# Optimization experiments

Hardware: AMD Instinct MI355X
Metric: run time of the kernel (lower is better)

The kernel has to match this reference:

```python
import jax, jax.numpy as jnp
import numpy as np

B, L, D = 2, 1024, 768
K = 64            # window_size
MLP_HIDDEN = 128
DIFF_STEPS = 1
EPS = 1e-8        # torch F.cosine_similarity eps


def setup_inputs() -> dict:
    key = jax.random.key(0)
    ks = jax.random.split(key, 7)
    x = jax.random.normal(ks[0], (B, L, D), dtype=jnp.float32)
    alpha = jnp.asarray(0.1, dtype=jnp.float32)
    pos_emb = jax.random.normal(ks[1], (K, D), dtype=jnp.float32) * 0.02
    w1 = jax.random.normal(ks[2], (2 * D, MLP_HIDDEN), dtype=jnp.float32) * 0.02
    b1 = jnp.zeros((MLP_HIDDEN,), dtype=jnp.float32)
    w2 = jax.random.normal(ks[3], (MLP_HIDDEN, D), dtype=jnp.float32) * 0.02
    b2 = jnp.zeros((D,), dtype=jnp.float32)
    return {"x": x, "alpha": alpha, "pos_emb": pos_emb,
            "w1": w1, "b1": b1, "w2": w2, "b2": b2}


def reference(x, alpha, pos_emb, w1, b1, w2, b2):
    Bx, Lx, Dx = x.shape
    W = Lx - K + 1  # number of sliding windows
    # gather indices for unfold(2, K, 1): window w covers positions [w, w+K)
    idx = jnp.arange(W)[:, None] + jnp.arange(K)[None, :]  # [W, K]

    x_curr = x
    first_pre_energy = jnp.asarray(0.0, jnp.float32)
    final_post_energy = jnp.asarray(0.0, jnp.float32)
    total_update_norm = jnp.asarray(0.0, jnp.float32)
    total_cos_sim = jnp.asarray(0.0, jnp.float32)

    for step in range(DIFF_STEPS):
        windows = x_curr[:, idx, :]                 # [B, W, K, D]
        context = windows[:, :, :-1, :]             # [B, W, K-1, D]
        current = windows[:, :, -1, :]              # [B, W, D]
        pe = jnp.broadcast_to(pos_emb[: K - 1], (Bx, W, K - 1, Dx))
        mlp_in = jnp.concatenate([context, pe], axis=-1)        # [B, W, K-1, 2D]
        h = jax.nn.relu(jnp.einsum('bwkc,ch->bwkh', mlp_in, w1) + b1)
        pred = jnp.einsum('bwkh,hd->bwkd', h, w2) + b2          # [B, W, K-1, D]
        deltas = current[:, :, None, :] - pred                  # [B, W, K-1, D]
        mean_delta = deltas.mean(axis=2)                        # [B, W, D]
        update = -(alpha * mean_delta)                          # [B, W, D]
        x_next = x_curr.at[:, K - 1:, :].add(update)

        pre_energy = (mean_delta ** 2).sum(axis=-1).mean()
        up_norm = jnp.linalg.norm(update, axis=-1).mean()
        a = current
        b = current + update
        na = jnp.maximum(jnp.linalg.norm(a, axis=-1), EPS)
        nb = jnp.maximum(jnp.linalg.norm(b, axis=-1), EPS)
        cos_sim = ((a * b).sum(axis=-1) / (na * nb)).mean()

        if step == 0:
            first_pre_energy = pre_energy
        total_update_norm = total_update_norm + up_norm
        total_cos_sim = total_cos_sim + cos_sim
        x_curr = x_next
        alpha_val = jax.lax.stop_gradient(alpha)  # mirrors .item() detach
        post_energy = (1.0 - alpha_val) ** 2 * pre_energy
        if step == DIFF_STEPS - 1:
            final_post_energy = post_energy

    return (x_curr,
            first_pre_energy,
            final_post_energy,
            total_update_norm / DIFF_STEPS,
            total_cos_sim / DIFF_STEPS)
```

## Files before the change

### kernel.cpp

```cpp
#include <hip/hip_runtime.h>

constexpr int Bn = 2;
constexpr int Ln = 1024;
constexpr int Dn = 768;
constexpr int Hn = 128;
constexpr int KM1 = 63;
constexpr int Wn = 961;
constexpr int RB = 4;
constexpr int WB = 8;
constexpr int WCHUNKS = (Wn + WB - 1) / WB;
constexpr int NROW = Bn * Wn;
constexpr float EPSf = 1e-8f;

__device__ __forceinline__ float4 f4l(const float* p) { return *reinterpret_cast<const float4*>(p); }
__device__ __forceinline__ void f4s(float* p, float4 v) { *reinterpret_cast<float4*>(p) = v; }
__device__ __forceinline__ float4 f4fma(float s, float4 w, float4 a) {
    a.x = fmaf(s, w.x, a.x); a.y = fmaf(s, w.y, a.y);
    a.z = fmaf(s, w.z, a.z); a.w = fmaf(s, w.w, a.w);
    return a;
}

__global__ __launch_bounds__(512)
void k_gemm1(const float* __restrict__ x, const float* __restrict__ pos_emb,
             const float* __restrict__ w1, const float* __restrict__ b1,
             float* __restrict__ xw1, float* __restrict__ pew1,
             float* __restrict__ out)
{
    __shared__ float xs[RB * Dn];
    __shared__ float part[16 * RB * Hn];
    const int tid = threadIdx.x;
    const int h4 = tid & 31;
    const int ks = tid >> 5;
    const int blk = blockIdx.x;
    constexpr int NXB = (Bn * Ln) / RB;
    const bool isX = blk < NXB;
    const int peb = blk - NXB;

    const float* src = isX ? (x + blk * RB * Dn) : (pos_emb + peb * RB * Dn);
    const int nv = isX ? RB : min(RB, KM1 - peb * RB);

    for (int idx = tid; idx < nv * (Dn / 4); idx += 512)
        ((float4*)xs)[idx] = ((const float4*)src)[idx];
    __syncthreads();

    if (isX) {
        const int r0 = blk * RB;
        if ((r0 & (Ln - 1)) < KM1) {
            for (int idx = tid; idx < RB * (Dn / 4); idx += 512) {
                const int i = idx / (Dn / 4);
                const int r = r0 + i;
                if ((r & (Ln - 1)) < KM1)
                    ((float4*)out)[r * (Dn / 4) + (idx - i * (Dn / 4))] = ((const float4*)xs)[idx];
            }
        }
    }

    const int woff = isX ? 0 : Dn;
    float4 acc0 = make_float4(0.f, 0.f, 0.f, 0.f);
    float4 acc1 = acc0, acc2 = acc0, acc3 = acc0;
    const int cbase = ks * 48;
    for (int cc = 0; cc < 48; cc += 4) {
        const int c = cbase + cc;
        const float* wp = w1 + (woff + c) * Hn + 4 * h4;
        const float4 wv0 = f4l(wp);
        const float4 wv1 = f4l(wp + Hn);
        const float4 wv2 = f4l(wp + 2 * Hn);
        const float4 wv3 = f4l(wp + 3 * Hn);
        const float4 x0 = ((const float4*)xs)[(0 * Dn + c) >> 2];
        const float4 x1 = ((const float4*)xs)[(1 * Dn + c) >> 2];
        const float4 x2 = ((const float4*)xs)[(2 * Dn + c) >> 2];
        const float4 x3 = ((const float4*)xs)[(3 * Dn + c) >> 2];
        acc0 = f4fma(x0.x, wv0, acc0); acc0 = f4fma(x0.y, wv1, acc0);
        acc0 = f4fma(x0.z, wv2, acc0); acc0 = f4fma(x0.w, wv3, acc0);
        acc1 = f4fma(x1.x, wv0, acc1); acc1 = f4fma(x1.y, wv1, acc1);
        acc1 = f4fma(x1.z, wv2, acc1); acc1 = f4fma(x1.w, wv3, acc1);
        acc2 = f4fma(x2.x, wv0, acc2); acc2 = f4fma(x2.y, wv1, acc2);
        acc2 = f4fma(x2.z, wv2, acc2); acc2 = f4fma(x2.w, wv3, acc2);
        acc3 = f4fma(x3.x, wv0, acc3); acc3 = f4fma(x3.y, wv1, acc3);
        acc3 = f4fma(x3.z, wv2, acc3); acc3 = f4fma(x3.w, wv3, acc3);
    }
    ((float4*)part)[((ks * RB + 0) * Hn + 4 * h4) >> 2] = acc0;
    ((float4*)part)[((ks * RB + 1) * Hn + 4 * h4) >> 2] = acc1;
    ((float4*)part)[((ks * RB + 2) * Hn + 4 * h4) >> 2] = acc2;
    ((float4*)part)[((ks * RB + 3) * Hn + 4 * h4) >> 2] = acc3;
    __syncthreads();

    const int oi = tid >> 7;
    const int oh = tid & 127;
    float s = 0.f;
    #pragma unroll
    for (int k2 = 0; k2 < 16; ++k2)
        s += part[(k2 * RB + oi) * Hn + oh];
    if (isX) {
        xw1[(blk * RB + oi) * Hn + oh] = s;
    } else if (oi < nv) {
        pew1[(peb * RB + oi) * Hn + oh] = s + b1[oh];
    }
}

__global__ __launch_bounds__(256)
void k_fused(const float* __restrict__ x, const float* __restrict__ alpha_p,
             const float* __restrict__ w2, const float* __restrict__ b2,
             const float* __restrict__ xw1, const float* __restrict__ pew1,
             float* __restrict__ out, float* __restrict__ partial)
{
    __shared__ float xsl[(WB + KM1 - 1) * Hn];
    __shared__ float hsm[WB * Hn];
    __shared__ float4 red[4 * WB * 64];
    const int tid = threadIdx.x;
    int bid = blockIdx.x;
    const int dc = bid % 3; bid /= 3;
    const int chunk = bid % WCHUNKS;
    const int b = bid / WCHUNKS;
    const int w0 = chunk * WB;
    const int wcount = min(WB, Wn - w0);
    const int nrows = wcount + KM1 - 1;
    const float alpha = alpha_p[0];

    {
        const float4* src = (const float4*)(xw1 + (b * Ln + w0) * Hn);
        for (int idx = tid; idx < nrows * (Hn / 4); idx += 256)
            ((float4*)xsl)[idx] = src[idx];
    }
    __syncthreads();

    {
        const int w = tid >> 5;
        const int h4 = tid & 31;
        float4 s = make_float4(0.f, 0.f, 0.f, 0.f);
        const float* pp = pew1 + 4 * h4;
        #pragma unroll 7
        for (int k = 0; k < KM1; ++k) {
            const float4 xv = ((const float4*)xsl)[((w + k) * Hn + 4 * h4) >> 2];
            const float4 pv = f4l(pp + k * Hn);
            s.x += fmaxf(xv.x + pv.x, 0.f);
            s.y += fmaxf(xv.y + pv.y, 0.f);
            s.z += fmaxf(xv.z + pv.z, 0.f);
            s.w += fmaxf(xv.w + pv.w, 0.f);
        }
        const float sc = 1.0f / 63.0f;
        s.x *= sc; s.y *= sc; s.z *= sc; s.w *= sc;
        ((float4*)hsm)[(w * Hn + 4 * h4) >> 2] = s;
    }
    __syncthreads();

    const int d4 = tid & 63;
    const int hs = tid >> 6;
    float4 acc[WB];
    #pragma unroll
    for (int w = 0; w < WB; ++w) acc[w] = make_float4(0.f, 0.f, 0.f, 0.f);
    const int d = dc * 256 + d4 * 4;
    const int h0 = hs * 32;
    for (int hh = 0; hh < 32; ++hh) {
        const int h = h0 + hh;
        const float4 wv = f4l(w2 + h * Dn + d);
        #pragma unroll
        for (int w = 0; w < WB; ++w)
            acc[w] = f4fma(hsm[w * Hn + h], wv, acc[w]);
    }
    #pragma unroll
    for (int w = 0; w < WB; ++w)
        red[(hs * WB + w) * 64 + d4] = acc[w];
    __syncthreads();

    const int wloc = tid >> 5;
    float4 pp = make_float4(0.f, 0.f, 0.f, 0.f);
    if (wloc < wcount) {
        const int rowoff = (b * Ln + w0 + wloc + KM1) * Dn + dc * 256;
        #pragma unroll
        for (int j = 0; j < 2; ++j) {
            const int dp = (2 * tid + j) & 63;
            float4 sum = red[wloc * 64 + dp];
            #pragma unroll
            for (int k = 1; k < 4; ++k) {
                const float4 u = red[(k * WB + wloc) * 64 + dp];
                sum.x += u.x; sum.y += u.y; sum.z += u.z; sum.w += u.w;
            }
            const float4 bb = f4l(b2 + dc * 256 + dp * 4);
            const float4 xv = f4l(x + rowoff + dp * 4);
            float4 md;
            md.x = xv.x - (sum.x + bb.x);
            md.y = xv.y - (sum.y + bb.y);
            md.z = xv.z - (sum.z + bb.z);
            md.w = xv.w - (sum.w + bb.w);
            float4 nb;
            nb.x = fmaf(-alpha, md.x, xv.x);
            nb.y = fmaf(-alpha, md.y, xv.y);
            nb.z = fmaf(-alpha, md.z, xv.z);
            nb.w = fmaf(-alpha, md.w, xv.w);
            f4s(out + rowoff + dp * 4, nb);
            pp.x += md.x * md.x + md.y * md.y + md.z * md.z + md.w * md.w;
            pp.y += xv.x * xv.x + xv.y * xv.y + xv.z * xv.z + xv.w * xv.w;
            pp.z += xv.x * nb.x + xv.y * nb.y + xv.z * nb.z + xv.w * nb.w;
            pp.w += nb.x * nb.x + nb.y * nb.y + nb.z * nb.z + nb.w * nb.w;
        }
    }
    #pragma unroll
    for (int off = 16; off > 0; off >>= 1) {
        pp.x += __shfl_xor(pp.x, off);
        pp.y += __shfl_xor(pp.y, off);
        pp.z += __shfl_xor(pp.z, off);
        pp.w += __shfl_xor(pp.w, off);
    }
    if (((tid & 31) == 0) && wloc < wcount)
        f4s(partial + (dc * NROW + b * Wn + w0 + wloc) * 4, pp);
}

__global__ __launch_bounds__(1024)
void k_final(const float* __restrict__ partial, const float* __restrict__ alpha_p,
             float* __restrict__ out)
{
    __shared__ float sred[16][3];
    const int tid = threadIdx.x;
    float se = 0.f, sn = 0.f, sc = 0.f;
    for (int r = tid; r < NROW; r += 1024) {
        const float4 v0 = ((const float4*)partial)[r];
        const float4 v1 = ((const float4*)partial)[NROW + r];
        const float4 v2 = ((const float4*)partial)[2 * NROW + r];
        const float sq = v0.x + v1.x + v2.x;
        const float aa = v0.y + v1.y + v2.y;
        const float ab = v0.z + v1.z + v2.z;
        const float bb = v0.w + v1.w + v2.w;
        se += sq;
        sn += sqrtf(sq);
        sc += ab / (fmaxf(sqrtf(aa), EPSf) * fmaxf(sqrtf(bb), EPSf));
    }
    #pragma unroll
    for (int off = 32; off > 0; off >>= 1) {
        se += __shfl_down(se, off);
        sn += __shfl_down(sn, off);
        sc += __shfl_down(sc, off);
    }
    const int wv = tid >> 6, lane = tid & 63;
    if (lane == 0) { sred[wv][0] = se; sred[wv][1] = sn; sred[wv][2] = sc; }
    __syncthreads();
    if (tid == 0) {
        float te = 0.f, tn = 0.f, tc = 0.f;
        #pragma unroll
        for (int i = 0; i < 16; ++i) {
            te += sred[i][0]; tn += sred[i][1]; tc += sred[i][2];
        }
        const float alpha = alpha_p[0];
        const float inv = 1.0f / (float)NROW;
        const float pre = te * inv;
        const float om = 1.0f - alpha;
        const int base = Bn * Ln * Dn;
        out[base + 0] = pre;
        out[base + 1] = om * om * pre;
        out[base + 2] = alpha * tn * inv;
        out[base + 3] = tc * inv;
    }
}

extern "C" void kernel_launch(void* const* d_in, const int* in_sizes, int n_in,
                              void* d_out, int out_size, void* d_ws, size_t ws_size,
                              hipStream_t stream)
{
    const float* x       = (const float*)d_in[0];
    const float* alpha_p = (const float*)d_in[1];
    const float* pos_emb = (const float*)d_in[2];
    const float* w1      = (const float*)d_in[3];
    const float* b1      = (const float*)d_in[4];
    const float* w2      = (const float*)d_in[5];
    const float* b2      = (const float*)d_in[6];
    float* out = (float*)d_out;

    float* xw1     = (float*)d_ws;
    float* pew1    = xw1 + Bn * Ln * Hn;
    float* partial = pew1 + KM1 * Hn;

    const int nblkA = (Bn * Ln) / RB + (KM1 + RB - 1) / RB;
    k_gemm1<<<nblkA, 512, 0, stream>>>(x, pos_emb, w1, b1, xw1, pew1, out);
    k_fused<<<Bn * WCHUNKS * 3, 256, 0, stream>>>(x, alpha_p, w2, b2, xw1, pew1, out, partial);
    k_final<<<1, 1024, 0, stream>>>(partial, alpha_p, out);
}
```

Measured before the change: 107.9 us.

## Fuse final reduction into main kernel via atomics and last-block completion

Drops the separate single-block final reduction kernel. The fused kernel now accumulates the energy, norm and cosine sums with global atomics, and the last block to finish (found through an atomic counter) writes the scalar outputs. Each block now covers all three D chunks for 4 windows instead of one chunk for 8, and the hidden-mean stage is split across k-groups with a shared-memory reduction. This removes one launch and the partial buffer, at the cost of atomic contention, float non-determinism in the sums, and a tiny grid for the W2 stage.

```diff
diff --git a/kernel.cpp b/kernel.cpp
--- a/kernel.cpp
+++ b/kernel.cpp
@@ -7,9 +7,10 @@
 constexpr int KM1 = 63;
 constexpr int Wn = 961;
 constexpr int RB = 4;
-constexpr int WB = 8;
+constexpr int WB = 4;
 constexpr int WCHUNKS = (Wn + WB - 1) / WB;
 constexpr int NROW = Bn * Wn;
+constexpr int FGRID = Bn * WCHUNKS;
 constexpr float EPSf = 1e-8f;
 
 __device__ __forceinline__ float4 f4l(const float* p) { return *reinterpret_cast<const float4*>(p); }
@@ -24,7 +25,7 @@
 void k_gemm1(const float* __restrict__ x, const float* __restrict__ pos_emb,
              const float* __restrict__ w1, const float* __restrict__ b1,
              float* __restrict__ xw1, float* __restrict__ pew1,
-             float* __restrict__ out)
+             float* __restrict__ out, float* __restrict__ accum)
 {
     __shared__ float xs[RB * Dn];
     __shared__ float part[16 * RB * Hn];
@@ -35,6 +36,8 @@
     constexpr int NXB = (Bn * Ln) / RB;
     const bool isX = blk < NXB;
     const int peb = blk - NXB;
+
+    if (blk == 0 && tid < 5) accum[tid] = 0.0f;
 
     const float* src = isX ? (x + blk * RB * Dn) : (pos_emb + peb * RB * Dn);
     const int nv = isX ? RB : min(RB, KM1 - peb * RB);
@@ -102,16 +105,16 @@
 void k_fused(const float* __restrict__ x, const float* __restrict__ alpha_p,
              const float* __restrict__ w2, const float* __restrict__ b2,
              const float* __restrict__ xw1, const float* __restrict__ pew1,
-             float* __restrict__ out, float* __restrict__ partial)
+             float* __restrict__ out, float* __restrict__ accum)
 {
     __shared__ float xsl[(WB + KM1 - 1) * Hn];
     __shared__ float hsm[WB * Hn];
-    __shared__ float4 red[4 * WB * 64];
+    __shared__ float4 red[1024];
+    __shared__ int lastFlag;
+
     const int tid = threadIdx.x;
-    int bid = blockIdx.x;
-    const int dc = bid % 3; bid /= 3;
-    const int chunk = bid % WCHUNKS;
-    const int b = bid / WCHUNKS;
+    const int b = blockIdx.x / WCHUNKS;
+    const int chunk = blockIdx.x % WCHUNKS;
     const int w0 = chunk * WB;
     const int wcount = min(WB, Wn - w0);
     const int nrows = wcount + KM1 - 1;
@@ -125,59 +128,77 @@
     __syncthreads();
 
     {
+        const int kg = tid >> 5;
+        const int h4 = tid & 31;
+        float4 s[WB];
+        #pragma unroll
+        for (int w = 0; w < WB; ++w) s[w] = make_float4(0.f, 0.f, 0.f, 0.f);
+        for (int k = kg; k < KM1; k += 8) {
+            const float4 pv = f4l(pew1 + k * Hn + 4 * h4);
+            #pragma unroll
+            for (int w = 0; w < WB; ++w) {
+                const float4 xv = ((const float4*)xsl)[((w + k) * Hn >> 2) + h4];
+                s[w].x += fmaxf(xv.x + pv.x, 0.f);
+                s[w].y += fmaxf(xv.y + pv.y, 0.f);
+                s[w].z += fmaxf(xv.z + pv.z, 0.f);
+                s[w].w += fmaxf(xv.w + pv.w, 0.f);
+            }
+        }
+        #pragma unroll
+        for (int w = 0; w < WB; ++w)
+            red[(kg * WB + w) * 32 + h4] = s[w];
+    }
+    __syncthreads();
+    if (tid < WB * 32) {
         const int w = tid >> 5;
         const int h4 = tid & 31;
-        float4 s = make_float4(0.f, 0.f, 0.f, 0.f);
-        const float* pp = pew1 + 4 * h4;
-        #pragma unroll 7
-        for (int k = 0; k < KM1; ++k) {
-            const float4 xv = ((const float4*)xsl)[((w + k) * Hn + 4 * h4) >> 2];
-            const float4 pv = f4l(pp + k * Hn);
-            s.x += fmaxf(xv.x + pv.x, 0.f);
-            s.y += fmaxf(xv.y + pv.y, 0.f);
-            s.z += fmaxf(xv.z + pv.z, 0.f);
-            s.w += fmaxf(xv.w + pv.w, 0.f);
+        float4 t = red[w * 32 + h4];
+        #pragma unroll
+        for (int kg = 1; kg < 8; ++kg) {
+            const float4 u = red[(kg * WB + w) * 32 + h4];
+            t.x += u.x; t.y += u.y; t.z += u.z; t.w += u.w;
         }
         const float sc = 1.0f / 63.0f;
-        s.x *= sc; s.y *= sc; s.z *= sc; s.w *= sc;
-        ((float4*)hsm)[(w * Hn + 4 * h4) >> 2] = s;
+        t.x *= sc; t.y *= sc; t.z *= sc; t.w *= sc;
+        ((float4*)hsm)[w * 32 + h4] = t;
     }
     __syncthreads();
 
     const int d4 = tid & 63;
     const int hs = tid >> 6;
-    float4 acc[WB];
-    #pragma unroll
-    for (int w = 0; w < WB; ++w) acc[w] = make_float4(0.f, 0.f, 0.f, 0.f);
-    const int d = dc * 256 + d4 * 4;
-    const int h0 = hs * 32;
-    for (int hh = 0; hh < 32; ++hh) {
-        const int h = h0 + hh;
-        const float4 wv = f4l(w2 + h * Dn + d);
+    const int wloc = hs;
+    float4 pp = make_float4(0.f, 0.f, 0.f, 0.f);
+
+    for (int dc = 0; dc < 3; ++dc) {
+        float4 acc[WB];
+        #pragma unroll
+        for (int w = 0; w < WB; ++w) acc[w] = make_float4(0.f, 0.f, 0.f, 0.f);
+        const int d = dc * 256 + d4 * 4;
+        const int h0 = hs * 32;
+        for (int hh = 0; hh < 32; ++hh) {
+            const int h = h0 + hh;
+            const float4 wv = f4l(w2 + h * Dn + d);
+            #pragma unroll
+            for (int w = 0; w < WB; ++w)
+                acc[w] = f4fma(hsm[w * Hn + h], wv, acc[w]);
+        }
+        __syncthreads();
         #pragma unroll
         for (int w = 0; w < WB; ++w)
-            acc[w] = f4fma(hsm[w * Hn + h], wv, acc[w]);
-    }
-    #pragma unroll
-    for (int w = 0; w < WB; ++w)
-        red[(hs * WB + w) * 64 + d4] = acc[w];
-    __syncthreads();
-
-    const int wloc = tid >> 5;
-    float4 pp = make_float4(0.f, 0.f, 0.f, 0.f);
-    if (wloc < wcount) {
-        const int rowoff = (b * Ln + w0 + wloc + KM1) * Dn + dc * 256;
-        #pragma unroll
-        for (int j = 0; j < 2; ++j) {
-            const int dp = (2 * tid + j) & 63;
-            float4 sum = red[wloc * 64 + dp];
+            red[(hs * WB + w) * 64 + d4] = acc[w];
+        __syncthreads();
+
+        if (wloc < wcount) {
+            const int row = b * Ln + w0 + wloc + KM1;
+            const int off = row * Dn + dc * 256 + d4 * 4;
+            float4 sum = red[wloc * 64 + d4];
             #pragma unroll
             for (int k = 1; k < 4; ++k) {
-                const float4 u = red[(k * WB + wloc) * 64 + dp];
+                const float4 u = red[(k * WB + wloc) * 64 + d4];
                 sum.x += u.x; sum.y += u.y; sum.z += u.z; sum.w += u.w;
             }
-            const float4 bb = f4l(b2 + dc * 256 + dp * 4);
-            const float4 xv = f4l(x + rowoff + dp * 4);
+            const float4 bb = f4l(b2 + dc * 256 + d4 * 4);
+            const float4 xv = f4l(x + off);
             float4 md;
             md.x = xv.x - (sum.x + bb.x);
             md.y = xv.y - (sum.y + bb.y);
@@ -188,67 +209,47 @@
             nb.y = fmaf(-alpha, md.y, xv.y);
             nb.z = fmaf(-alpha, md.z, xv.z);
             nb.w = fmaf(-alpha, md.w, xv.w);
-            f4s(out + rowoff + dp * 4, nb);
+            f4s(out + off, nb);
             pp.x += md.x * md.x + md.y * md.y + md.z * md.z + md.w * md.w;
             pp.y += xv.x * xv.x + xv.y * xv.y + xv.z * xv.z + xv.w * xv.w;
             pp.z += xv.x * nb.x + xv.y * nb.y + xv.z * nb.z + xv.w * nb.w;
             pp.w += nb.x * nb.x + nb.y * nb.y + nb.z * nb.z + nb.w * nb.w;
         }
     }
+
     #pragma unroll
-    for (int off = 16; off > 0; off >>= 1) {
+    for (int off = 32; off > 0; off >>= 1) {
         pp.x += __shfl_xor(pp.x, off);
         pp.y += __shfl_xor(pp.y, off);
         pp.z += __shfl_xor(pp.z, off);
         pp.w += __shfl_xor(pp.w, off);
     }
-    if (((tid & 31) == 0) && wloc < wcount)
-        f4s(partial + (dc * NROW + b * Wn + w0 + wloc) * 4, pp);
-}
-
-__global__ __launch_bounds__(1024)
-void k_final(const float* __restrict__ partial, const float* __restrict__ alpha_p,
-             float* __restrict__ out)
-{
-    __shared__ float sred[16][3];
-    const int tid = threadIdx.x;
-    float se = 0.f, sn = 0.f, sc = 0.f;
-    for (int r = tid; r < NROW; r += 1024) {
-        const float4 v0 = ((const float4*)partial)[r];
-        const float4 v1 = ((const float4*)partial)[NROW + r];
-        const float4 v2 = ((const float4*)partial)[2 * NROW + r];
-        const float sq = v0.x + v1.x + v2.x;
-        const float aa = v0.y + v1.y + v2.y;
-        const float ab = v0.z + v1.z + v2.z;
-        const float bb = v0.w + v1.w + v2.w;
-        se += sq;
-        sn += sqrtf(sq);
-        sc += ab / (fmaxf(sqrtf(aa), EPSf) * fmaxf(sqrtf(bb), EPSf));
-    }
-    #pragma unroll
-    for (int off = 32; off > 0; off >>= 1) {
-        se += __shfl_down(se, off);
-        sn += __shfl_down(sn, off);
-        sc += __shfl_down(sc, off);
-    }
-    const int wv = tid >> 6, lane = tid & 63;
-    if (lane == 0) { sred[wv][0] = se; sred[wv][1] = sn; sred[wv][2] = sc; }
-    __syncthreads();
+    if ((tid & 63) == 0 && wloc < wcount) {
+        atomicAdd(&accum[0], pp.x);
+        atomicAdd(&accum[1], sqrtf(pp.x));
+        atomicAdd(&accum[2], pp.z / (fmaxf(sqrtf(pp.y), EPSf) *
+                                     fmaxf(sqrtf(pp.w), EPSf)));
+    }
+    __syncthreads();
+
     if (tid == 0) {
-        float te = 0.f, tn = 0.f, tc = 0.f;
-        #pragma unroll
-        for (int i = 0; i < 16; ++i) {
-            te += sred[i][0]; tn += sred[i][1]; tc += sred[i][2];
-        }
-        const float alpha = alpha_p[0];
+        __threadfence();
+        const int old = atomicAdd((int*)(accum + 4), 1);
+        lastFlag = (old == FGRID - 1) ? 1 : 0;
+    }
+    __syncthreads();
+    if (lastFlag && tid == 0) {
+        const float se = atomicAdd(&accum[0], 0.0f);
+        const float sn = atomicAdd(&accum[1], 0.0f);
+        const float sc = atomicAdd(&accum[2], 0.0f);
         const float inv = 1.0f / (float)NROW;
-        const float pre = te * inv;
+        const float pre = se * inv;
         const float om = 1.0f - alpha;
         const int base = Bn * Ln * Dn;
         out[base + 0] = pre;
         out[base + 1] = om * om * pre;
-        out[base + 2] = alpha * tn * inv;
-        out[base + 3] = tc * inv;
+        out[base + 2] = alpha * sn * inv;
+        out[base + 3] = sc * inv;
     }
 }
 
@@ -265,12 +266,11 @@
     const float* b2      = (const float*)d_in[6];
     float* out = (float*)d_out;
 
-    float* xw1     = (float*)d_ws;
-    float* pew1    = xw1 + Bn * Ln * Hn;
-    float* partial = pew1 + KM1 * Hn;
+    float* xw1   = (float*)d_ws;
+    float* pew1  = xw1 + Bn * Ln * Hn;
+    float* accum = pew1 + KM1 * Hn;
 
     const int nblkA = (Bn * Ln) / RB + (KM1 + RB - 1) / RB;
-    k_gemm1<<<nblkA, 512, 0, stream>>>(x, pos_emb, w1, b1, xw1, pew1, out);
-    k_fused<<<Bn * WCHUNKS * 3, 256, 0, stream>>>(x, alpha_p, w2, b2, xw1, pew1, out, partial);
-    k_final<<<1, 1024, 0, stream>>>(partial, alpha_p, out);
-}
+    k_gemm1<<<nblkA, 512, 0, stream>>>(x, pos_emb, w1, b1, xw1, pew1, out, accum);
+    k_fused<<<FGRID, 256, 0, stream>>>(x, alpha_p, w2, b2, xw1, pew1, out, accum);
+}
```

New measurement: 176.4 us. +63.5%, slower.

## Fuse final reduction via atomic ticket, split GEMM1 across H halves, restructure ReLU-sum

Applied to the files above, without the earlier changes.

Drops the separate final reduction kernel. Per-row statistics are now accumulated with atomics into a workspace that the first kernel zeroes, and a last-block ticket runs the global reduction. The first GEMM is split into two blocks per row group, each covering half of the hidden dimension, with a padded shared-memory partial buffer. The windowed ReLU sum now has each warp own a slice of window offsets with pos-embedding values held in registers, followed by a cross-warp reduction. The second GEMM is also unrolled by four. This saves a launch and improves parallelism, at the cost of atomic contention, a pew1 read past row 62 (row 63 is loaded but unused), and reliance on the ticket counter being reset each call.

```diff
diff --git a/kernel.cpp b/kernel.cpp
--- a/kernel.cpp
+++ b/kernel.cpp
@@ -6,11 +6,18 @@
 constexpr int Hn = 128;
 constexpr int KM1 = 63;
 constexpr int Wn = 961;
-constexpr int RB = 4;
-constexpr int WB = 8;
-constexpr int WCHUNKS = (Wn + WB - 1) / WB;
 constexpr int NROW = Bn * Wn;
 constexpr float EPSf = 1e-8f;
+
+constexpr int RB1 = 4;
+constexpr int NXG = (Bn * Ln) / RB1;
+constexpr int NPEG = 16;
+constexpr int G1 = (NXG + NPEG) * 2;
+constexpr int PSTR = 66;
+
+constexpr int WB = 8;
+constexpr int WCH = (Wn + WB - 1) / WB;
+constexpr int FG = Bn * WCH * 3;
 
 __device__ __forceinline__ float4 f4l(const float* p) { return *reinterpret_cast<const float4*>(p); }
 __device__ __forceinline__ void f4s(float* p, float4 v) { *reinterpret_cast<float4*>(p) = v; }
@@ -24,29 +31,32 @@
 void k_gemm1(const float* __restrict__ x, const float* __restrict__ pos_emb,
              const float* __restrict__ w1, const float* __restrict__ b1,
              float* __restrict__ xw1, float* __restrict__ pew1,
-             float* __restrict__ out)
+             float* __restrict__ out, float* __restrict__ rowacc)
 {
-    __shared__ float xs[RB * Dn];
-    __shared__ float part[16 * RB * Hn];
+    __shared__ float xs[RB1 * Dn];
+    __shared__ float part[32 * RB1 * PSTR];
     const int tid = threadIdx.x;
-    const int h4 = tid & 31;
-    const int ks = tid >> 5;
     const int blk = blockIdx.x;
-    constexpr int NXB = (Bn * Ln) / RB;
-    const bool isX = blk < NXB;
-    const int peb = blk - NXB;
-
-    const float* src = isX ? (x + blk * RB * Dn) : (pos_emb + peb * RB * Dn);
-    const int nv = isX ? RB : min(RB, KM1 - peb * RB);
+    const int grp = blk >> 1;
+    const int hh  = blk & 1;
+    const bool isX = grp < NXG;
+    const int pg = grp - NXG;
+
+    if (blk == 0) {
+        for (int i = tid; i < NROW * 4 + 1; i += 512) rowacc[i] = 0.0f;
+    }
+
+    const float* src = isX ? (x + grp * RB1 * Dn) : (pos_emb + pg * RB1 * Dn);
+    const int nv = isX ? RB1 : min(RB1, KM1 - pg * RB1);
 
     for (int idx = tid; idx < nv * (Dn / 4); idx += 512)
         ((float4*)xs)[idx] = ((const float4*)src)[idx];
     __syncthreads();
 
-    if (isX) {
-        const int r0 = blk * RB;
+    if (isX && hh == 0) {
+        const int r0 = grp * RB1;
         if ((r0 & (Ln - 1)) < KM1) {
-            for (int idx = tid; idx < RB * (Dn / 4); idx += 512) {
+            for (int idx = tid; idx < RB1 * (Dn / 4); idx += 512) {
                 const int i = idx / (Dn / 4);
                 const int r = r0 + i;
                 if ((r & (Ln - 1)) < KM1)
@@ -55,13 +65,17 @@
         }
     }
 
+    const int h4 = tid & 15;
+    const int ks = tid >> 4;
     const int woff = isX ? 0 : Dn;
-    float4 acc0 = make_float4(0.f, 0.f, 0.f, 0.f);
-    float4 acc1 = acc0, acc2 = acc0, acc3 = acc0;
-    const int cbase = ks * 48;
-    for (int cc = 0; cc < 48; cc += 4) {
-        const int c = cbase + cc;
-        const float* wp = w1 + (woff + c) * Hn + 4 * h4;
+    const int hbase = hh * 64 + 4 * h4;
+    float4 a0 = make_float4(0.f, 0.f, 0.f, 0.f);
+    float4 a1 = a0, a2 = a0, a3 = a0;
+    const int c0 = ks * 24;
+    #pragma unroll
+    for (int cc = 0; cc < 24; cc += 4) {
+        const int c = c0 + cc;
+        const float* wp = w1 + (woff + c) * Hn + hbase;
         const float4 wv0 = f4l(wp);
         const float4 wv1 = f4l(wp + Hn);
         const float4 wv2 = f4l(wp + 2 * Hn);
@@ -70,31 +84,40 @@
         const float4 x1 = ((const float4*)xs)[(1 * Dn + c) >> 2];
         const float4 x2 = ((const float4*)xs)[(2 * Dn + c) >> 2];
         const float4 x3 = ((const float4*)xs)[(3 * Dn + c) >> 2];
-        acc0 = f4fma(x0.x, wv0, acc0); acc0 = f4fma(x0.y, wv1, acc0);
-        acc0 = f4fma(x0.z, wv2, acc0); acc0 = f4fma(x0.w, wv3, acc0);
-        acc1 = f4fma(x1.x, wv0, acc1); acc1 = f4fma(x1.y, wv1, acc1);
-        acc1 = f4fma(x1.z, wv2, acc1); acc1 = f4fma(x1.w, wv3, acc1);
-        acc2 = f4fma(x2.x, wv0, acc2); acc2 = f4fma(x2.y, wv1, acc2);
-        acc2 = f4fma(x2.z, wv2, acc2); acc2 = f4fma(x2.w, wv3, acc2);
-        acc3 = f4fma(x3.x, wv0, acc3); acc3 = f4fma(x3.y, wv1, acc3);
-        acc3 = f4fma(x3.z, wv2, acc3); acc3 = f4fma(x3.w, wv3, acc3);
-    }
-    ((float4*)part)[((ks * RB + 0) * Hn + 4 * h4) >> 2] = acc0;
-    ((float4*)part)[((ks * RB + 1) * Hn + 4 * h4) >> 2] = acc1;
-    ((float4*)part)[((ks * RB + 2) * Hn + 4 * h4) >> 2] = acc2;
-    ((float4*)part)[((ks * RB + 3) * Hn + 4 * h4) >> 2] = acc3;
-    __syncthreads();
-
-    const int oi = tid >> 7;
-    const int oh = tid & 127;
-    float s = 0.f;
-    #pragma unroll
-    for (int k2 = 0; k2 < 16; ++k2)
-        s += part[(k2 * RB + oi) * Hn + oh];
-    if (isX) {
-        xw1[(blk * RB + oi) * Hn + oh] = s;
-    } else if (oi < nv) {
-        pew1[(peb * RB + oi) * Hn + oh] = s + b1[oh];
+        a0 = f4fma(x0.x, wv0, a0); a0 = f4fma(x0.y, wv1, a0);
+        a0 = f4fma(x0.z, wv2, a0); a0 = f4fma(x0.w, wv3, a0);
+        a1 = f4fma(x1.x, wv0, a1); a1 = f4fma(x1.y, wv1, a1);
+        a1 = f4fma(x1.z, wv2, a1); a1 = f4fma(x1.w, wv3, a1);
+        a2 = f4fma(x2.x, wv0, a2); a2 = f4fma(x2.y, wv1, a2);
+        a2 = f4fma(x2.z, wv2, a2); a2 = f4fma(x2.w, wv3, a2);
+        a3 = f4fma(x3.x, wv0, a3); a3 = f4fma(x3.y, wv1, a3);
+        a3 = f4fma(x3.z, wv2, a3); a3 = f4fma(x3.w, wv3, a3);
+    }
+    {
+        const int hb = 4 * h4;
+        float* p0 = part + (ks * RB1 + 0) * PSTR + hb;
+        float* p1 = part + (ks * RB1 + 1) * PSTR + hb;
+        float* p2 = part + (ks * RB1 + 2) * PSTR + hb;
+        float* p3 = part + (ks * RB1 + 3) * PSTR + hb;
+        p0[0] = a0.x; p0[1] = a0.y; p0[2] = a0.z; p0[3] = a0.w;
+        p1[0] = a1.x; p1[1] = a1.y; p1[2] = a1.z; p1[3] = a1.w;
+        p2[0] = a2.x; p2[1] = a2.y; p2[2] = a2.z; p2[3] = a2.w;
+        p3[0] = a3.x; p3[1] = a3.y; p3[2] = a3.z; p3[3] = a3.w;
+    }
+    __syncthreads();
+
+    if (tid < 256) {
+        const int r = tid >> 6;
+        const int hloc = tid & 63;
+        float s = 0.f;
+        #pragma unroll
+        for (int k2 = 0; k2 < 32; ++k2)
+            s += part[(k2 * RB1 + r) * PSTR + hloc];
+        if (isX) {
+            xw1[(grp * RB1 + r) * Hn + hh * 64 + hloc] = s;
+        } else if (r < nv) {
+            pew1[(pg * RB1 + r) * Hn + hh * 64 + hloc] = s + b1[hh * 64 + hloc];
+        }
     }
 }
 
@@ -102,20 +125,23 @@
 void k_fused(const float* __restrict__ x, const float* __restrict__ alpha_p,
              const float* __restrict__ w2, const float* __restrict__ b2,
              const float* __restrict__ xw1, const float* __restrict__ pew1,
-             float* __restrict__ out, float* __restrict__ partial)
+             float* __restrict__ out, float* __restrict__ rowacc)
 {
     __shared__ float xsl[(WB + KM1 - 1) * Hn];
     __shared__ float hsm[WB * Hn];
     __shared__ float4 red[4 * WB * 64];
+    __shared__ int lastFlag;
+
     const int tid = threadIdx.x;
     int bid = blockIdx.x;
     const int dc = bid % 3; bid /= 3;
-    const int chunk = bid % WCHUNKS;
-    const int b = bid / WCHUNKS;
+    const int chunk = bid % WCH;
+    const int b = bid / WCH;
     const int w0 = chunk * WB;
     const int wcount = min(WB, Wn - w0);
     const int nrows = wcount + KM1 - 1;
     const float alpha = alpha_p[0];
+    int* ticket = (int*)(rowacc + NROW * 4);
 
     {
         const float4* src = (const float4*)(xw1 + (b * Ln + w0) * Hn);
@@ -125,22 +151,44 @@
     __syncthreads();
 
     {
+        const int kg = tid >> 5;
+        const int h4 = tid & 31;
+        float4 pv[8];
+        #pragma unroll
+        for (int j = 0; j < 8; ++j)
+            pv[j] = f4l(pew1 + (kg * 8 + j) * Hn + 4 * h4);
+        const int nj = (kg == 7) ? 7 : 8;
+        float4 s[WB];
+        #pragma unroll
+        for (int w = 0; w < WB; ++w) s[w] = make_float4(0.f, 0.f, 0.f, 0.f);
+        for (int j = 0; j < nj; ++j) {
+            const int k = kg * 8 + j;
+            #pragma unroll
+            for (int w = 0; w < WB; ++w) {
+                const float4 xv = ((const float4*)xsl)[(w + k) * (Hn / 4) + h4];
+                s[w].x += fmaxf(xv.x + pv[j].x, 0.f);
+                s[w].y += fmaxf(xv.y + pv[j].y, 0.f);
+                s[w].z += fmaxf(xv.z + pv[j].z, 0.f);
+                s[w].w += fmaxf(xv.w + pv[j].w, 0.f);
+            }
+        }
+        #pragma unroll
+        for (int w = 0; w < WB; ++w)
+            red[(kg * WB + w) * 32 + h4] = s[w];
+    }
+    __syncthreads();
+    {
         const int w = tid >> 5;
         const int h4 = tid & 31;
-        float4 s = make_float4(0.f, 0.f, 0.f, 0.f);
-        const float* pp = pew1 + 4 * h4;
-        #pragma unroll 7
-        for (int k = 0; k < KM1; ++k) {
-            const float4 xv = ((const float4*)xsl)[((w + k) * Hn + 4 * h4) >> 2];
-            const float4 pv = f4l(pp + k * Hn);
-            s.x += fmaxf(xv.x + pv.x, 0.f);
-            s.y += fmaxf(xv.y + pv.y, 0.f);
-            s.z += fmaxf(xv.z + pv.z, 0.f);
-            s.w += fmaxf(xv.w + pv.w, 0.f);
+        float4 t = red[w * 32 + h4];
+        #pragma unroll
+        for (int kg = 1; kg < 8; ++kg) {
+            const float4 u = red[(kg * WB + w) * 32 + h4];
+            t.x += u.x; t.y += u.y; t.z += u.z; t.w += u.w;
         }
         const float sc = 1.0f / 63.0f;
-        s.x *= sc; s.y *= sc; s.z *= sc; s.w *= sc;
-        ((float4*)hsm)[(w * Hn + 4 * h4) >> 2] = s;
+        t.x *= sc; t.y *= sc; t.z *= sc; t.w *= sc;
+        ((float4*)hsm)[w * 32 + h4] = t;
     }
     __syncthreads();
 
@@ -149,14 +197,23 @@
     float4 acc[WB];
     #pragma unroll
     for (int w = 0; w < WB; ++w) acc[w] = make_float4(0.f, 0.f, 0.f, 0.f);
-    const int d = dc * 256 + d4 * 4;
-    const int h0 = hs * 32;
-    for (int hh = 0; hh < 32; ++hh) {
-        const int h = h0 + hh;
-        const float4 wv = f4l(w2 + h * Dn + d);
-        #pragma unroll
-        for (int w = 0; w < WB; ++w)
-            acc[w] = f4fma(hsm[w * Hn + h], wv, acc[w]);
+    {
+        const float* wbase = w2 + (hs * 32) * Dn + dc * 256 + d4 * 4;
+        #pragma unroll
+        for (int t = 0; t < 8; ++t) {
+            const float4 wv0 = f4l(wbase + (4 * t + 0) * Dn);
+            const float4 wv1 = f4l(wbase + (4 * t + 1) * Dn);
+            const float4 wv2 = f4l(wbase + (4 * t + 2) * Dn);
+            const float4 wv3 = f4l(wbase + (4 * t + 3) * Dn);
+            const int h = hs * 32 + 4 * t;
+            #pragma unroll
+            for (int w = 0; w < WB; ++w) {
+                acc[w] = f4fma(hsm[w * Hn + h + 0], wv0, acc[w]);
+                acc[w] = f4fma(hsm[w * Hn + h + 1], wv1, acc[w]);
+                acc[w] = f4fma(hsm[w * Hn + h + 2], wv2, acc[w]);
+                acc[w] = f4fma(hsm[w * Hn + h + 3], wv3, acc[w]);
+            }
+        }
     }
     #pragma unroll
     for (int w = 0; w < WB; ++w)
@@ -194,61 +251,63 @@
             pp.z += xv.x * nb.x + xv.y * nb.y + xv.z * nb.z + xv.w * nb.w;
             pp.w += nb.x * nb.x + nb.y * nb.y + nb.z * nb.z + nb.w * nb.w;
         }
-    }
-    #pragma unroll
-    for (int off = 16; off > 0; off >>= 1) {
-        pp.x += __shfl_xor(pp.x, off);
-        pp.y += __shfl_xor(pp.y, off);
-        pp.z += __shfl_xor(pp.z, off);
-        pp.w += __shfl_xor(pp.w, off);
-    }
-    if (((tid & 31) == 0) && wloc < wcount)
-        f4s(partial + (dc * NROW + b * Wn + w0 + wloc) * 4, pp);
-}
-
-__global__ __launch_bounds__(1024)
-void k_final(const float* __restrict__ partial, const float* __restrict__ alpha_p,
-             float* __restrict__ out)
-{
-    __shared__ float sred[16][3];
-    const int tid = threadIdx.x;
-    float se = 0.f, sn = 0.f, sc = 0.f;
-    for (int r = tid; r < NROW; r += 1024) {
-        const float4 v0 = ((const float4*)partial)[r];
-        const float4 v1 = ((const float4*)partial)[NROW + r];
-        const float4 v2 = ((const float4*)partial)[2 * NROW + r];
-        const float sq = v0.x + v1.x + v2.x;
-        const float aa = v0.y + v1.y + v2.y;
-        const float ab = v0.z + v1.z + v2.z;
-        const float bb = v0.w + v1.w + v2.w;
-        se += sq;
-        sn += sqrtf(sq);
-        sc += ab / (fmaxf(sqrtf(aa), EPSf) * fmaxf(sqrtf(bb), EPSf));
-    }
-    #pragma unroll
-    for (int off = 32; off > 0; off >>= 1) {
-        se += __shfl_down(se, off);
-        sn += __shfl_down(sn, off);
-        sc += __shfl_down(sc, off);
-    }
-    const int wv = tid >> 6, lane = tid & 63;
-    if (lane == 0) { sred[wv][0] = se; sred[wv][1] = sn; sred[wv][2] = sc; }
-    __syncthreads();
+        #pragma unroll
+        for (int off = 16; off > 0; off >>= 1) {
+            pp.x += __shfl_xor(pp.x, off);
+            pp.y += __shfl_xor(pp.y, off);
+            pp.z += __shfl_xor(pp.z, off);
+            pp.w += __shfl_xor(pp.w, off);
+        }
+        if ((tid & 31) == 0) {
+            float* ra = rowacc + (b * Wn + w0 + wloc) * 4;
+            atomicAdd(ra + 0, pp.x);
+            atomicAdd(ra + 1, pp.y);
+            atomicAdd(ra + 2, pp.z);
+            atomicAdd(ra + 3, pp.w);
+        }
+    }
+    __syncthreads();
+
     if (tid == 0) {
-        float te = 0.f, tn = 0.f, tc = 0.f;
-        #pragma unroll
-        for (int i = 0; i < 16; ++i) {
-            te += sred[i][0]; tn += sred[i][1]; tc += sred[i][2];
-        }
-        const float alpha = alpha_p[0];
-        const float inv = 1.0f / (float)NROW;
-        const float pre = te * inv;
-        const float om = 1.0f - alpha;
-        const int base = Bn * Ln * Dn;
-        out[base + 0] = pre;
-        out[base + 1] = om * om * pre;
-        out[base + 2] = alpha * tn * inv;
-        out[base + 3] = tc * inv;
+        __threadfence();
+        const int old = atomicAdd(ticket, 1);
+        lastFlag = (old == FG - 1) ? 1 : 0;
+    }
+    __syncthreads();
+    if (lastFlag) {
+        __threadfence();
+        float se = 0.f, sn = 0.f, sc = 0.f;
+        for (int r = tid; r < NROW; r += 256) {
+            const float4 v = f4l(rowacc + r * 4);
+            se += v.x;
+            sn += sqrtf(v.x);
+            sc += v.z / (fmaxf(sqrtf(v.y), EPSf) * fmaxf(sqrtf(v.w), EPSf));
+        }
+        #pragma unroll
+        for (int off = 32; off > 0; off >>= 1) {
+            se += __shfl_down(se, off);
+            sn += __shfl_down(sn, off);
+            sc += __shfl_down(sc, off);
+        }
+        float* rs = (float*)red;
+        const int wv = tid >> 6, lane = tid & 63;
+        if (lane == 0) { rs[wv * 3 + 0] = se; rs[wv * 3 + 1] = sn; rs[wv * 3 + 2] = sc; }
+        __syncthreads();
+        if (tid == 0) {
+            float te = 0.f, tn = 0.f, tc = 0.f;
+            #pragma unroll
+            for (int i = 0; i < 4; ++i) {
+                te += rs[i * 3 + 0]; tn += rs[i * 3 + 1]; tc += rs[i * 3 + 2];
+            }
+            const float inv = 1.0f / (float)NROW;
+            const float pre = te * inv;
+            const float om = 1.0f - alpha;
+            const int base = Bn * Ln * Dn;
+            out[base + 0] = pre;
+            out[base + 1] = om * om * pre;
+            out[base + 2] = alpha * tn * inv;
+            out[base + 3] = tc * inv;
+        }
     }
 }
 
@@ -265,12 +324,10 @@
     const float* b2      = (const float*)d_in[6];
     float* out = (float*)d_out;
 
-    float* xw1     = (float*)d_ws;
-    float* pew1    = xw1 + Bn * Ln * Hn;
-    float* partial = pew1 + KM1 * Hn;
-
-    const int nblkA = (Bn * Ln) / RB + (KM1 + RB - 1) / RB;
-    k_gemm1<<<nblkA, 512, 0, stream>>>(x, pos_emb, w1, b1, xw1, pew1, out);
-    k_fused<<<Bn * WCHUNKS * 3, 256, 0, stream>>>(x, alpha_p, w2, b2, xw1, pew1, out, partial);
-    k_final<<<1, 1024, 0, stream>>>(partial, alpha_p, out);
+    float* xw1    = (float*)d_ws;
+    float* pew1   = xw1 + Bn * Ln * Hn;
+    float* rowacc = pew1 + 64 * Hn;
+
+    k_gemm1<<<G1, 512, 0, stream>>>(x, pos_emb, w1, b1, xw1, pew1, out, rowacc);
+    k_fused<<<FG, 256, 0, stream>>>(x, alpha_p, w2, b2, xw1, pew1, out, rowacc);
 }
```

Result: slower. 136.3 us (+26.3%).
